# Performance work log

Measured on AMD Instinct MI355X. Metric: run time of the kernel, lower is better.

Reference implementation:

```python
import jax, jax.numpy as jnp
import numpy as np

NUM_HEADS = 16
NUM_GROUPS = 2
HEAD_DIM = 128  # in_features // num_heads = 2048 // 16
MAX_POS = 512 + 256 + 256  # MAX_SEQ_LEN + SHARED_SLOTS + OUTPUT_SLOTS


def _rope_tables():
    inv_freq = 1.0 / 10000 ** (jnp.arange(0, HEAD_DIM, 2) / HEAD_DIM)
    t = jnp.arange(MAX_POS)
    freqs = jnp.outer(t, inv_freq)
    freqs = jnp.concatenate([freqs, freqs], axis=-1)  # [MAX_POS, HEAD_DIM]
    return jnp.sin(freqs), jnp.cos(freqs)


def _rotate_half(x):
    h = x.shape[-1] // 2
    x1, x2 = x[..., :h], x[..., h:]
    return jnp.concatenate([-x2, x1], axis=-1)


def setup_inputs() -> dict:
    key = jax.random.key(0)
    ks = jax.random.split(key, 5)
    b, s, d = 4, 1024, 2048
    kvd = NUM_GROUPS * HEAD_DIM
    sc = 1.0 / np.sqrt(d).astype(np.float32)
    return {
        "x": jax.random.normal(ks[0], (b, s, d), jnp.float32),
        "Wq": jax.random.normal(ks[1], (d, d), jnp.float32) * sc,
        "bq": jnp.zeros((d,), jnp.float32),
        "Wk": jax.random.normal(ks[2], (d, kvd), jnp.float32) * sc,
        "bk": jnp.zeros((kvd,), jnp.float32),
        "Wv": jax.random.normal(ks[3], (d, kvd), jnp.float32) * sc,
        "bv": jnp.zeros((kvd,), jnp.float32),
        "Wo": jax.random.normal(ks[4], (d, d), jnp.float32) * sc,
        "bo": jnp.zeros((d,), jnp.float32),
    }


def reference(x, Wq, bq, Wk, bk, Wv, bv, Wo, bo):
    b, s, d = x.shape
    sin, cos = _rope_tables()
    # original: sin_cached[q_pos, None, :] broadcasts over (b, s, heads, head_dim)
    sin = sin[:s][None, :, None, :]
    cos = cos[:s][None, :, None, :]

    q = (x @ Wq + bq).reshape(b, s, NUM_HEADS, HEAD_DIM)
    k = (x @ Wk + bk).reshape(b, s, NUM_GROUPS, HEAD_DIM)
    v = (x @ Wv + bv).reshape(b, s, NUM_GROUPS, HEAD_DIM)

    q = q * cos + _rotate_half(q) * sin
    k = k * cos + _rotate_half(k) * sin

    # GQA: avoid materializing expanded K/V by grouping the head dim of q.
    r = NUM_HEADS // NUM_GROUPS  # repeats per group
    qg = q.reshape(b, s, NUM_GROUPS, r, HEAD_DIM)
    scale = HEAD_DIM ** -0.5
    scores = jnp.einsum('bsgrd,btgd->bgrst', qg, k) * scale
    attn = jax.nn.softmax(scores, axis=-1)
    out = jnp.einsum('bgrst,btgd->bsgrd', attn, v).reshape(b, s, d)
    return out @ Wo + bo
```

## Files before the change

### kernel.cpp

```cpp
#include <hip/hip_runtime.h>
#include <hip/hip_bf16.h>
#include <hip/hip_fp16.h>
#include <math.h>

#define BATCH   4
#define SEQ     1024
#define DMODEL  2048
#define NHEADS  16
#define NGROUPS 2
#define HDIM    128
#define ROWS    (BATCH * SEQ)
#define NQKV    2560

typedef float    f32x4 __attribute__((ext_vector_type(4)));
typedef _Float16 f16x8 __attribute__((ext_vector_type(8)));

__device__ __forceinline__ void glds16(const void* g, void* s) {
    __builtin_amdgcn_global_load_lds(
        (__attribute__((address_space(1))) void*)g,
        (__attribute__((address_space(3))) void*)s, 16, 0, 0);
}

__global__ void rope_table_kernel(float* __restrict__ sin_t, float* __restrict__ cos_t) {
    int idx = blockIdx.x * 256 + threadIdx.x;
    int p = idx >> 6, j = idx & 63;
    float inv = powf(10000.0f, -(float)j * (1.0f / 64.0f));
    float f = (float)p * inv;
    sin_t[idx] = sinf(f);
    cos_t[idx] = cosf(f);
}

__global__ void convert_x_kernel(const float* __restrict__ x, _Float16* __restrict__ xo) {
    int i = (blockIdx.x * 256 + threadIdx.x) * 8;
    float v[8];
    *reinterpret_cast<float4*>(&v[0]) = *reinterpret_cast<const float4*>(x + i);
    *reinterpret_cast<float4*>(&v[4]) = *reinterpret_cast<const float4*>(x + i + 4);
    f16x8 h;
#pragma unroll
    for (int j = 0; j < 8; ++j) h[j] = (_Float16)v[j];
    *reinterpret_cast<f16x8*>(xo + i) = h;
}

__global__ __launch_bounds__(256)
void transpose_w_kernel(const float* __restrict__ W, int ldw,
                        _Float16* __restrict__ dst, int drow0, int K) {
    __shared__ float tile[64][65];
    int n0 = blockIdx.x * 64, k0 = blockIdx.y * 64;
#pragma unroll
    for (int it = 0; it < 16; ++it) {
        int e = it * 256 + threadIdx.x;
        int r = e >> 6, c = e & 63;
        tile[r][c] = W[(size_t)(k0 + r) * ldw + n0 + c];
    }
    __syncthreads();
#pragma unroll
    for (int it = 0; it < 16; ++it) {
        int e = it * 256 + threadIdx.x;
        int nr = e >> 6, kc = e & 63;
        dst[(size_t)(drow0 + n0 + nr) * K + k0 + kc] = (_Float16)tile[kc][nr];
    }
}

__global__ void bias_cat_kernel(const float* __restrict__ bq, const float* __restrict__ bk,
                                const float* __restrict__ bv, float* __restrict__ bc) {
    int i = blockIdx.x * 256 + threadIdx.x;
    if (i >= NQKV) return;
    bc[i] = (i < 2048) ? bq[i] : ((i < 2304) ? bk[i - 2048] : bv[i - 2304]);
}

template<int OUT_HALF>
__global__ __launch_bounds__(256, 3)
void gemm_fp16_kernel(const _Float16* __restrict__ A, const _Float16* __restrict__ Bt,
                      const float* __restrict__ bias, void* __restrict__ Cout,
                      int M, int N, int K) {
    __shared__ __align__(16) _Float16 lds[16384];
    _Float16* As = lds;
    _Float16* Bs = lds + 8192;

    const int tid  = threadIdx.x;
    const int lane = tid & 63;
    const int w    = tid >> 6;
    const int nbn  = N >> 7;
    const int nwg  = gridDim.x;
    const int cpx  = nwg >> 3;
    const int bid  = blockIdx.x;
    const int swz  = (bid & 7) * cpx + (bid >> 3);
    const int row0 = (swz / nbn) << 7;
    const int col0 = (swz % nbn) << 7;
    const int wr   = (w >> 1) << 6;
    const int wc   = (w & 1) << 6;

    const f32x4 fz = {0.f, 0.f, 0.f, 0.f};
    f32x4 acc[4][4];
#pragma unroll
    for (int i = 0; i < 4; ++i)
#pragma unroll
        for (int j = 0; j < 4; ++j) acc[i][j] = fz;

    for (int k0 = 0; k0 < K; k0 += 64) {
        __syncthreads();
#pragma unroll
        for (int it = 0; it < 4; ++it) {
            int chunk = it * 256 + tid;
            int trow  = chunk >> 3;
            int jp    = chunk & 7;
            int j     = jp ^ (trow & 7);
            size_t aoff = (size_t)(row0 + trow) * K + k0 + j * 8;
            size_t boff = (size_t)(col0 + trow) * K + k0 + j * 8;
            int ldst = (it * 256 + (tid & 192)) * 16;
            glds16(A  + aoff, (char*)As + ldst);
            glds16(Bt + boff, (char*)Bs + ldst);
        }
        __syncthreads();

#pragma unroll
        for (int ks = 0; ks < 2; ++ks) {
            f16x8 a4[4], b4[4];
            int ja = ks * 4 + (lane >> 4);
#pragma unroll
            for (int i = 0; i < 4; ++i) {
                int ar = wr + i * 16 + (lane & 15);
                a4[i] = *reinterpret_cast<const f16x8*>(
                    (const char*)As + ar * 128 + ((ja ^ (ar & 7)) << 4));
                int br = wc + i * 16 + (lane & 15);
                b4[i] = *reinterpret_cast<const f16x8*>(
                    (const char*)Bs + br * 128 + ((ja ^ (br & 7)) << 4));
            }
#pragma unroll
            for (int i = 0; i < 4; ++i)
#pragma unroll
                for (int j = 0; j < 4; ++j)
                    acc[i][j] = __builtin_amdgcn_mfma_f32_16x16x32_f16(a4[i], b4[j], acc[i][j], 0, 0, 0);
        }
    }

    float bv4[4];
#pragma unroll
    for (int j = 0; j < 4; ++j) bv4[j] = bias[col0 + wc + j * 16 + (lane & 15)];
#pragma unroll
    for (int i = 0; i < 4; ++i)
#pragma unroll
        for (int j = 0; j < 4; ++j)
#pragma unroll
            for (int r = 0; r < 4; ++r) {
                int grow = row0 + wr + i * 16 + ((lane >> 4) << 2) + r;
                int gcol = col0 + wc + j * 16 + (lane & 15);
                float v = acc[i][j][r] + bv4[j];
                if (OUT_HALF)
                    ((_Float16*)Cout)[(size_t)grow * N + gcol] = (_Float16)v;
                else
                    ((float*)Cout)[(size_t)grow * N + gcol] = v;
            }
}

__global__ void rope_k_kernel(const _Float16* __restrict__ qkv,
                              const float* __restrict__ sin_t, const float* __restrict__ cos_t,
                              _Float16* __restrict__ kh) {
    int idx = blockIdx.x * 256 + threadIdx.x;
    int jc = idx & 7, t = idx >> 3;
    int j0 = jc * 8;
    int row = t >> 1, g = t & 1;
    int b = row >> 10, s = row & 1023;
    const _Float16* src = qkv + (size_t)row * NQKV + 2048 + g * HDIM;
    _Float16* dst = kh + ((size_t)(b * NGROUPS + g) * SEQ + s) * HDIM;
    f16x8 x1 = *reinterpret_cast<const f16x8*>(src + j0);
    f16x8 x2 = *reinterpret_cast<const f16x8*>(src + j0 + 64);
    float cc[8], ss[8];
    *reinterpret_cast<float4*>(&cc[0]) = *reinterpret_cast<const float4*>(cos_t + s * 64 + j0);
    *reinterpret_cast<float4*>(&cc[4]) = *reinterpret_cast<const float4*>(cos_t + s * 64 + j0 + 4);
    *reinterpret_cast<float4*>(&ss[0]) = *reinterpret_cast<const float4*>(sin_t + s * 64 + j0);
    *reinterpret_cast<float4*>(&ss[4]) = *reinterpret_cast<const float4*>(sin_t + s * 64 + j0 + 4);
    f16x8 o1, o2;
#pragma unroll
    for (int j = 0; j < 8; ++j) {
        float f1 = (float)x1[j], f2 = (float)x2[j];
        o1[j] = (_Float16)(f1 * cc[j] - f2 * ss[j]);
        o2[j] = (_Float16)(f2 * cc[j] + f1 * ss[j]);
    }
    *reinterpret_cast<f16x8*>(dst + j0)      = o1;
    *reinterpret_cast<f16x8*>(dst + j0 + 64) = o2;
}

__global__ __launch_bounds__(256)
void transpose_v_kernel(const _Float16* __restrict__ qkv, _Float16* __restrict__ vt) {
    __shared__ _Float16 tile[64][72];
    int s0 = blockIdx.x * 64, d0 = blockIdx.y * 64, bg = blockIdx.z;
    int b = bg >> 1, g = bg & 1;
#pragma unroll
    for (int it = 0; it < 2; ++it) {
        int c = it * 256 + threadIdx.x;
        int r = c >> 3, cc = (c & 7) * 8;
        f16x8 v = *reinterpret_cast<const f16x8*>(
            qkv + (size_t)(b * SEQ + s0 + r) * NQKV + 2304 + g * HDIM + d0 + cc);
#pragma unroll
        for (int j = 0; j < 8; ++j) tile[r][cc + j] = v[j];
    }
    __syncthreads();
#pragma unroll
    for (int it = 0; it < 2; ++it) {
        int c = it * 256 + threadIdx.x;
        int dr = c >> 3, sc = (c & 7) * 8;
        f16x8 o;
#pragma unroll
        for (int j = 0; j < 8; ++j) o[j] = tile[sc + j][dr];
        *reinterpret_cast<f16x8*>(vt + ((size_t)bg * HDIM + d0 + dr) * SEQ + s0 + sc) = o;
    }
}

__global__ __launch_bounds__(256, 2)
void attn_kernel(const _Float16* __restrict__ qkv, const _Float16* __restrict__ kh,
                 const _Float16* __restrict__ vt,
                 const float* __restrict__ sin_t, const float* __restrict__ cos_t,
                 _Float16* __restrict__ ao) {
    __shared__ __align__(16) char smem[73728];

    const int tid = threadIdx.x, lane = tid & 63, w = tid >> 6;
    const int qt0 = blockIdx.x << 6;
    const int h = blockIdx.y, b = blockIdx.z;
    const int g = h >> 3;
    const _Float16* kbase = kh + (size_t)(b * NGROUPS + g) * SEQ * HDIM;
    const _Float16* vbase = vt + (size_t)(b * NGROUPS + g) * HDIM * SEQ;

    {
        char* Kb = smem;
        char* Vb = smem + 16384;
#pragma unroll
        for (int it = 0; it < 4; ++it) {
            int c = it * 256 + tid;
            int row = c >> 4, jc = c & 15;
            int sj = jc ^ (row & 7);
            glds16((const char*)(kbase + (size_t)row * HDIM) + (sj << 4),
                   Kb + (it * 256 + (tid & 192)) * 16);
        }
#pragma unroll
        for (int it = 0; it < 4; ++it) {
            int c = it * 256 + tid;
            int d = c >> 3, jc = c & 7;
            int sj = jc ^ (d & 7);
            glds16((const char*)(vbase + (size_t)d * SEQ) + (sj << 4),
                   Vb + (it * 256 + (tid & 192)) * 16);
        }
    }

    const int srow = qt0 + w * 16 + (lane & 15);
    const int sl   = lane >> 4;
    const _Float16* qrp = qkv + (size_t)(b * SEQ + srow) * NQKV + h * HDIM;
    f16x8 af[4];
#pragma unroll
    for (int ks = 0; ks < 4; ++ks)
        af[ks] = *reinterpret_cast<const f16x8*>(qrp + (ks * 4 + sl) * 8);
    {
        const float qsc = 0.08838834764831845f;
#pragma unroll
        for (int ks = 0; ks < 2; ++ks) {
            int d0 = (ks * 4 + sl) * 8;
            float cc[8], ss[8];
            *reinterpret_cast<float4*>(&cc[0]) = *reinterpret_cast<const float4*>(cos_t + srow * 64 + d0);
            *reinterpret_cast<float4*>(&cc[4]) = *reinterpret_cast<const float4*>(cos_t + srow * 64 + d0 + 4);
            *reinterpret_cast<float4*>(&ss[0]) = *reinterpret_cast<const float4*>(sin_t + srow * 64 + d0);
            *reinterpret_cast<float4*>(&ss[4]) = *reinterpret_cast<const float4*>(sin_t + srow * 64 + d0 + 4);
#pragma unroll
            for (int j = 0; j < 8; ++j) {
                float f1 = (float)af[ks][j], f2 = (float)af[ks + 2][j];
                af[ks][j]     = (_Float16)((f1 * cc[j] - f2 * ss[j]) * qsc);
                af[ks + 2][j] = (_Float16)((f2 * cc[j] + f1 * ss[j]) * qsc);
            }
        }
    }

    float m_run[4] = {-1e30f, -1e30f, -1e30f, -1e30f};
    float l_run[4] = {0.f, 0.f, 0.f, 0.f};
    const f32x4 fz = {0.f, 0.f, 0.f, 0.f};
    f32x4 oacc[8];
#pragma unroll
    for (int i = 0; i < 8; ++i) oacc[i] = fz;

    char* Pw = smem + 65536 + w * 2048;
    const int prow = lane & 15;
    const int pswz = prow & 7;

    int cur = 0;
    for (int t = 0; t < SEQ / 64; ++t) {
        char* Kb = smem + (cur << 15);
        char* Vb = Kb + 16384;
        if (t < SEQ / 64 - 1) {
            char* Kn = smem + ((cur ^ 1) << 15);
            char* Vn = Kn + 16384;
            int t0n = (t + 1) << 6;
#pragma unroll
            for (int it = 0; it < 4; ++it) {
                int c = it * 256 + tid;
                int row = c >> 4, jc = c & 15;
                int sj = jc ^ (row & 7);
                glds16((const char*)(kbase + (size_t)(t0n + row) * HDIM) + (sj << 4),
                       Kn + (it * 256 + (tid & 192)) * 16);
            }
#pragma unroll
            for (int it = 0; it < 4; ++it) {
                int c = it * 256 + tid;
                int d = c >> 3, jc = c & 7;
                int sj = jc ^ (d & 7);
                glds16((const char*)(vbase + (size_t)d * SEQ + t0n) + (sj << 4),
                       Vn + (it * 256 + (tid & 192)) * 16);
            }
            asm volatile("s_waitcnt vmcnt(8)" ::: "memory");
        } else {
            asm volatile("s_waitcnt vmcnt(0)" ::: "memory");
        }
        asm volatile("s_barrier" ::: "memory");

        f32x4 sacc[4];
#pragma unroll
        for (int i = 0; i < 4; ++i) sacc[i] = fz;
#pragma unroll
        for (int ks = 0; ks < 4; ++ks) {
#pragma unroll
            for (int nf = 0; nf < 4; ++nf) {
                int trow = nf * 16 + (lane & 15);
                f16x8 bf = *reinterpret_cast<const f16x8*>(
                    Kb + trow * 256 + (((ks * 4 + (lane >> 4)) ^ (trow & 7)) << 4));
                sacc[nf] = __builtin_amdgcn_mfma_f32_16x16x32_f16(af[ks], bf, sacc[nf], 0, 0, 0);
            }
        }

        float pm[4];
#pragma unroll
        for (int r = 0; r < 4; ++r) {
            float v = fmaxf(fmaxf(sacc[0][r], sacc[1][r]), fmaxf(sacc[2][r], sacc[3][r]));
            v = fmaxf(v, __shfl_xor(v, 1, 16));
            v = fmaxf(v, __shfl_xor(v, 2, 16));
            v = fmaxf(v, __shfl_xor(v, 4, 16));
            v = fmaxf(v, __shfl_xor(v, 8, 16));
            pm[r] = v;
        }
        float growth = fmaxf(fmaxf(pm[0] - m_run[0], pm[1] - m_run[1]),
                             fmaxf(pm[2] - m_run[2], pm[3] - m_run[3]));
        if (__any(growth > 8.0f)) {
            float scl[4];
#pragma unroll
            for (int r = 0; r < 4; ++r) {
                float mn = fmaxf(m_run[r], pm[r]);
                scl[r] = __expf(m_run[r] - mn);
                m_run[r] = mn;
                l_run[r] *= scl[r];
            }
#pragma unroll
            for (int i = 0; i < 8; ++i) {
                f32x4 o = oacc[i];
                o[0] *= scl[0]; o[1] *= scl[1]; o[2] *= scl[2]; o[3] *= scl[3];
                oacc[i] = o;
            }
        }
        float psum[4] = {0.f, 0.f, 0.f, 0.f};
#pragma unroll
        for (int nf = 0; nf < 4; ++nf)
#pragma unroll
            for (int r = 0; r < 4; ++r) {
                float p = __expf(sacc[nf][r] - m_run[r]);
                sacc[nf][r] = p;
                psum[r] += p;
            }
#pragma unroll
        for (int r = 0; r < 4; ++r) {
            float ps = psum[r];
            ps += __shfl_xor(ps, 1, 16);
            ps += __shfl_xor(ps, 2, 16);
            ps += __shfl_xor(ps, 4, 16);
            ps += __shfl_xor(ps, 8, 16);
            l_run[r] += ps;
        }

#pragma unroll
        for (int nf = 0; nf < 4; ++nf)
#pragma unroll
            for (int r = 0; r < 4; ++r) {
                int pr = ((lane >> 4) << 2) + r;
                int pc = nf * 16 + (lane & 15);
                int byte = pr * 128 + ((pc * 2) ^ ((pr & 7) << 4));
                *reinterpret_cast<_Float16*>(Pw + byte) = (_Float16)sacc[nf][r];
            }

#pragma unroll
        for (int ks = 0; ks < 2; ++ks) {
            int chP = ks * 4 + (lane >> 4);
            f16x8 pa = *reinterpret_cast<const f16x8*>(Pw + prow * 128 + ((chP ^ pswz) << 4));
#pragma unroll
            for (int nf = 0; nf < 8; ++nf) {
                int vrow = nf * 16 + (lane & 15);
                f16x8 vf = *reinterpret_cast<const f16x8*>(
                    Vb + vrow * 128 + (((ks * 4 + (lane >> 4)) ^ (vrow & 7)) << 4));
                oacc[nf] = __builtin_amdgcn_mfma_f32_16x16x32_f16(pa, vf, oacc[nf], 0, 0, 0);
            }
        }

        asm volatile("s_barrier" ::: "memory");
        cur ^= 1;
    }

#pragma unroll
    for (int nf = 0; nf < 8; ++nf)
#pragma unroll
        for (int r = 0; r < 4; ++r) {
            int qr  = qt0 + w * 16 + ((lane >> 4) << 2) + r;
            int col = h * HDIM + nf * 16 + (lane & 15);
            float v = oacc[nf][r] / l_run[r];
            ao[(size_t)(b * SEQ + qr) * DMODEL + col] = (_Float16)v;
        }
}

extern "C" void kernel_launch(void* const* d_in, const int* in_sizes, int n_in,
                              void* d_out, int out_size, void* d_ws, size_t ws_size,
                              hipStream_t stream) {
    const float* x  = (const float*)d_in[0];
    const float* Wq = (const float*)d_in[1];
    const float* bq = (const float*)d_in[2];
    const float* Wk = (const float*)d_in[3];
    const float* bk = (const float*)d_in[4];
    const float* Wv = (const float*)d_in[5];
    const float* bv = (const float*)d_in[6];
    const float* Wo = (const float*)d_in[7];
    const float* bo = (const float*)d_in[8];
    float* out = (float*)d_out;

    char* ws = (char*)d_ws;
    _Float16* xs     = (_Float16*)(ws);
    _Float16* wqkv16 = (_Float16*)(ws + 16777216);
    _Float16* wot16  = (_Float16*)(ws + 27262976);
    _Float16* qkv16  = (_Float16*)(ws + 35651584);
    _Float16* khb    = (_Float16*)(ws + 56623104);
    _Float16* vtb    = (_Float16*)(ws + 58720256);
    float*    sint   = (float*)(ws + 60817408);
    float*    cost   = (float*)(ws + 61079552);
    float*    bias_c = (float*)(ws + 61341696);
    _Float16* ao = xs;

    rope_table_kernel<<<SEQ * 64 / 256, 256, 0, stream>>>(sint, cost);
    convert_x_kernel<<<ROWS * DMODEL / 8 / 256, 256, 0, stream>>>(x, xs);
    transpose_w_kernel<<<dim3(32, 32), 256, 0, stream>>>(Wq, DMODEL, wqkv16, 0, DMODEL);
    transpose_w_kernel<<<dim3(4, 32),  256, 0, stream>>>(Wk, 256,    wqkv16, 2048, DMODEL);
    transpose_w_kernel<<<dim3(4, 32),  256, 0, stream>>>(Wv, 256,    wqkv16, 2304, DMODEL);
    transpose_w_kernel<<<dim3(32, 32), 256, 0, stream>>>(Wo, DMODEL, wot16,  0, DMODEL);
    bias_cat_kernel<<<10, 256, 0, stream>>>(bq, bk, bv, bias_c);

    gemm_fp16_kernel<1><<<(ROWS / 128) * (NQKV / 128), 256, 0, stream>>>(
        xs, wqkv16, bias_c, qkv16, ROWS, NQKV, DMODEL);

    rope_k_kernel<<<(ROWS * NGROUPS * 8) / 256, 256, 0, stream>>>(qkv16, sint, cost, khb);
    transpose_v_kernel<<<dim3(SEQ / 64, HDIM / 64, BATCH * NGROUPS), 256, 0, stream>>>(qkv16, vtb);

    attn_kernel<<<dim3(SEQ / 64, NHEADS, BATCH), 256, 0, stream>>>(
        qkv16, khb, vtb, sint, cost, ao);

    gemm_fp16_kernel<0><<<(ROWS / 128) * (DMODEL / 128), 256, 0, stream>>>(
        ao, wot16, bo, out, ROWS, DMODEL, DMODEL);
}
```

Measured before the change: 318.9 us.

## Process 32 query rows per wave in attention and use DPP row reductions

Each attention block now covers 128 query rows, with each wave holding two 16-row Q fragments, so every K and V fragment read from LDS feeds two MFMAs. The grid is halved and the per-wave P buffer is doubled in size. The 16-lane max and sum reductions now use DPP moves instead of shuffles. In exchange, the larger accumulator set raises register pressure, and the smaller grid may reduce occupancy and SM coverage.

```diff
diff --git a/kernel.cpp b/kernel.cpp
--- a/kernel.cpp
+++ b/kernel.cpp
@@ -19,6 +19,21 @@
     __builtin_amdgcn_global_load_lds(
         (__attribute__((address_space(1))) void*)g,
         (__attribute__((address_space(3))) void*)s, 16, 0, 0);
+}
+
+__device__ __forceinline__ float red16_max(float v) {
+    v = fmaxf(v, __int_as_float(__builtin_amdgcn_mov_dpp(__float_as_int(v), 0xB1, 0xF, 0xF, true)));
+    v = fmaxf(v, __int_as_float(__builtin_amdgcn_mov_dpp(__float_as_int(v), 0x4E, 0xF, 0xF, true)));
+    v = fmaxf(v, __int_as_float(__builtin_amdgcn_mov_dpp(__float_as_int(v), 0x124, 0xF, 0xF, true)));
+    v = fmaxf(v, __int_as_float(__builtin_amdgcn_mov_dpp(__float_as_int(v), 0x128, 0xF, 0xF, true)));
+    return v;
+}
+__device__ __forceinline__ float red16_sum(float v) {
+    v += __int_as_float(__builtin_amdgcn_mov_dpp(__float_as_int(v), 0xB1, 0xF, 0xF, true));
+    v += __int_as_float(__builtin_amdgcn_mov_dpp(__float_as_int(v), 0x4E, 0xF, 0xF, true));
+    v += __int_as_float(__builtin_amdgcn_mov_dpp(__float_as_int(v), 0x124, 0xF, 0xF, true));
+    v += __int_as_float(__builtin_amdgcn_mov_dpp(__float_as_int(v), 0x128, 0xF, 0xF, true));
+    return v;
 }
 
 __global__ void rope_table_kernel(float* __restrict__ sin_t, float* __restrict__ cos_t) {
@@ -212,10 +227,10 @@
                  const _Float16* __restrict__ vt,
                  const float* __restrict__ sin_t, const float* __restrict__ cos_t,
                  _Float16* __restrict__ ao) {
-    __shared__ __align__(16) char smem[73728];
+    __shared__ __align__(16) char smem[81920];
 
     const int tid = threadIdx.x, lane = tid & 63, w = tid >> 6;
-    const int qt0 = blockIdx.x << 6;
+    const int qt0 = blockIdx.x << 7;
     const int h = blockIdx.y, b = blockIdx.z;
     const int g = h >> 3;
     const _Float16* kbase = kh + (size_t)(b * NGROUPS + g) * SEQ * HDIM;
@@ -242,14 +257,15 @@
         }
     }
 
-    const int srow = qt0 + w * 16 + (lane & 15);
-    const int sl   = lane >> 4;
-    const _Float16* qrp = qkv + (size_t)(b * SEQ + srow) * NQKV + h * HDIM;
-    f16x8 af[4];
-#pragma unroll
-    for (int ks = 0; ks < 4; ++ks)
-        af[ks] = *reinterpret_cast<const f16x8*>(qrp + (ks * 4 + sl) * 8);
-    {
+    const int sl = lane >> 4;
+    f16x8 af[2][4];
+#pragma unroll
+    for (int m = 0; m < 2; ++m) {
+        int srow = qt0 + w * 32 + m * 16 + (lane & 15);
+        const _Float16* qrp = qkv + (size_t)(b * SEQ + srow) * NQKV + h * HDIM;
+#pragma unroll
+        for (int ks = 0; ks < 4; ++ks)
+            af[m][ks] = *reinterpret_cast<const f16x8*>(qrp + (ks * 4 + sl) * 8);
         const float qsc = 0.08838834764831845f;
 #pragma unroll
         for (int ks = 0; ks < 2; ++ks) {
@@ -261,23 +277,27 @@
             *reinterpret_cast<float4*>(&ss[4]) = *reinterpret_cast<const float4*>(sin_t + srow * 64 + d0 + 4);
 #pragma unroll
             for (int j = 0; j < 8; ++j) {
-                float f1 = (float)af[ks][j], f2 = (float)af[ks + 2][j];
-                af[ks][j]     = (_Float16)((f1 * cc[j] - f2 * ss[j]) * qsc);
-                af[ks + 2][j] = (_Float16)((f2 * cc[j] + f1 * ss[j]) * qsc);
-            }
-        }
-    }
-
-    float m_run[4] = {-1e30f, -1e30f, -1e30f, -1e30f};
-    float l_run[4] = {0.f, 0.f, 0.f, 0.f};
+                float f1 = (float)af[m][ks][j], f2 = (float)af[m][ks + 2][j];
+                af[m][ks][j]     = (_Float16)((f1 * cc[j] - f2 * ss[j]) * qsc);
+                af[m][ks + 2][j] = (_Float16)((f2 * cc[j] + f1 * ss[j]) * qsc);
+            }
+        }
+    }
+
+    float m_run[2][4], l_run[2][4];
+#pragma unroll
+    for (int m = 0; m < 2; ++m)
+#pragma unroll
+        for (int r = 0; r < 4; ++r) { m_run[m][r] = -1e30f; l_run[m][r] = 0.f; }
     const f32x4 fz = {0.f, 0.f, 0.f, 0.f};
-    f32x4 oacc[8];
-#pragma unroll
-    for (int i = 0; i < 8; ++i) oacc[i] = fz;
-
-    char* Pw = smem + 65536 + w * 2048;
+    f32x4 oacc[2][8];
+#pragma unroll
+    for (int m = 0; m < 2; ++m)
+#pragma unroll
+        for (int i = 0; i < 8; ++i) oacc[m][i] = fz;
+
+    char* Pw = smem + 65536 + w * 4096;
     const int prow = lane & 15;
-    const int pswz = prow & 7;
 
     int cur = 0;
     for (int t = 0; t < SEQ / 64; ++t) {
@@ -309,9 +329,11 @@
         }
         asm volatile("s_barrier" ::: "memory");
 
-        f32x4 sacc[4];
-#pragma unroll
-        for (int i = 0; i < 4; ++i) sacc[i] = fz;
+        f32x4 sacc[2][4];
+#pragma unroll
+        for (int m = 0; m < 2; ++m)
+#pragma unroll
+            for (int i = 0; i < 4; ++i) sacc[m][i] = fz;
 #pragma unroll
         for (int ks = 0; ks < 4; ++ks) {
 #pragma unroll
@@ -319,77 +341,85 @@
                 int trow = nf * 16 + (lane & 15);
                 f16x8 bf = *reinterpret_cast<const f16x8*>(
                     Kb + trow * 256 + (((ks * 4 + (lane >> 4)) ^ (trow & 7)) << 4));
-                sacc[nf] = __builtin_amdgcn_mfma_f32_16x16x32_f16(af[ks], bf, sacc[nf], 0, 0, 0);
-            }
-        }
-
-        float pm[4];
-#pragma unroll
-        for (int r = 0; r < 4; ++r) {
-            float v = fmaxf(fmaxf(sacc[0][r], sacc[1][r]), fmaxf(sacc[2][r], sacc[3][r]));
-            v = fmaxf(v, __shfl_xor(v, 1, 16));
-            v = fmaxf(v, __shfl_xor(v, 2, 16));
-            v = fmaxf(v, __shfl_xor(v, 4, 16));
-            v = fmaxf(v, __shfl_xor(v, 8, 16));
-            pm[r] = v;
-        }
-        float growth = fmaxf(fmaxf(pm[0] - m_run[0], pm[1] - m_run[1]),
-                             fmaxf(pm[2] - m_run[2], pm[3] - m_run[3]));
+                sacc[0][nf] = __builtin_amdgcn_mfma_f32_16x16x32_f16(af[0][ks], bf, sacc[0][nf], 0, 0, 0);
+                sacc[1][nf] = __builtin_amdgcn_mfma_f32_16x16x32_f16(af[1][ks], bf, sacc[1][nf], 0, 0, 0);
+            }
+        }
+
+        float pm[2][4];
+        float growth = -1e30f;
+#pragma unroll
+        for (int m = 0; m < 2; ++m)
+#pragma unroll
+            for (int r = 0; r < 4; ++r) {
+                float v = fmaxf(fmaxf(sacc[m][0][r], sacc[m][1][r]),
+                                fmaxf(sacc[m][2][r], sacc[m][3][r]));
+                v = red16_max(v);
+                pm[m][r] = v;
+                growth = fmaxf(growth, v - m_run[m][r]);
+            }
         if (__any(growth > 8.0f)) {
-            float scl[4];
+            float scl[2][4];
+#pragma unroll
+            for (int m = 0; m < 2; ++m)
+#pragma unroll
+                for (int r = 0; r < 4; ++r) {
+                    float mn = fmaxf(m_run[m][r], pm[m][r]);
+                    scl[m][r] = __expf(m_run[m][r] - mn);
+                    m_run[m][r] = mn;
+                    l_run[m][r] *= scl[m][r];
+                }
+#pragma unroll
+            for (int m = 0; m < 2; ++m)
+#pragma unroll
+                for (int i = 0; i < 8; ++i) {
+                    f32x4 o = oacc[m][i];
+                    o[0] *= scl[m][0]; o[1] *= scl[m][1];
+                    o[2] *= scl[m][2]; o[3] *= scl[m][3];
+                    oacc[m][i] = o;
+                }
+        }
+#pragma unroll
+        for (int m = 0; m < 2; ++m)
 #pragma unroll
             for (int r = 0; r < 4; ++r) {
-                float mn = fmaxf(m_run[r], pm[r]);
-                scl[r] = __expf(m_run[r] - mn);
-                m_run[r] = mn;
-                l_run[r] *= scl[r];
-            }
-#pragma unroll
-            for (int i = 0; i < 8; ++i) {
-                f32x4 o = oacc[i];
-                o[0] *= scl[0]; o[1] *= scl[1]; o[2] *= scl[2]; o[3] *= scl[3];
-                oacc[i] = o;
-            }
-        }
-        float psum[4] = {0.f, 0.f, 0.f, 0.f};
-#pragma unroll
-        for (int nf = 0; nf < 4; ++nf)
-#pragma unroll
-            for (int r = 0; r < 4; ++r) {
-                float p = __expf(sacc[nf][r] - m_run[r]);
-                sacc[nf][r] = p;
-                psum[r] += p;
-            }
-#pragma unroll
-        for (int r = 0; r < 4; ++r) {
-            float ps = psum[r];
-            ps += __shfl_xor(ps, 1, 16);
-            ps += __shfl_xor(ps, 2, 16);
-            ps += __shfl_xor(ps, 4, 16);
-            ps += __shfl_xor(ps, 8, 16);
-            l_run[r] += ps;
-        }
-
-#pragma unroll
-        for (int nf = 0; nf < 4; ++nf)
-#pragma unroll
-            for (int r = 0; r < 4; ++r) {
-                int pr = ((lane >> 4) << 2) + r;
-                int pc = nf * 16 + (lane & 15);
-                int byte = pr * 128 + ((pc * 2) ^ ((pr & 7) << 4));
-                *reinterpret_cast<_Float16*>(Pw + byte) = (_Float16)sacc[nf][r];
-            }
+                float ps = 0.f;
+#pragma unroll
+                for (int nf = 0; nf < 4; ++nf) {
+                    float p = __expf(sacc[m][nf][r] - m_run[m][r]);
+                    sacc[m][nf][r] = p;
+                    ps += p;
+                }
+                l_run[m][r] += red16_sum(ps);
+            }
+
+#pragma unroll
+        for (int m = 0; m < 2; ++m)
+#pragma unroll
+            for (int nf = 0; nf < 4; ++nf)
+#pragma unroll
+                for (int r = 0; r < 4; ++r) {
+                    int pr = m * 16 + ((lane >> 4) << 2) + r;
+                    int pc = nf * 16 + (lane & 15);
+                    int byte = pr * 128 + ((pc * 2) ^ ((pr & 7) << 4));
+                    *reinterpret_cast<_Float16*>(Pw + byte) = (_Float16)sacc[m][nf][r];
+                }
 
 #pragma unroll
         for (int ks = 0; ks < 2; ++ks) {
             int chP = ks * 4 + (lane >> 4);
-            f16x8 pa = *reinterpret_cast<const f16x8*>(Pw + prow * 128 + ((chP ^ pswz) << 4));
+            f16x8 pa[2];
+#pragma unroll
+            for (int m = 0; m < 2; ++m)
+                pa[m] = *reinterpret_cast<const f16x8*>(
+                    Pw + (m * 16 + prow) * 128 + ((chP ^ (prow & 7)) << 4));
 #pragma unroll
             for (int nf = 0; nf < 8; ++nf) {
                 int vrow = nf * 16 + (lane & 15);
                 f16x8 vf = *reinterpret_cast<const f16x8*>(
                     Vb + vrow * 128 + (((ks * 4 + (lane >> 4)) ^ (vrow & 7)) << 4));
-                oacc[nf] = __builtin_amdgcn_mfma_f32_16x16x32_f16(pa, vf, oacc[nf], 0, 0, 0);
+                oacc[0][nf] = __builtin_amdgcn_mfma_f32_16x16x32_f16(pa[0], vf, oacc[0][nf], 0, 0, 0);
+                oacc[1][nf] = __builtin_amdgcn_mfma_f32_16x16x32_f16(pa[1], vf, oacc[1][nf], 0, 0, 0);
             }
         }
 
@@ -398,14 +428,16 @@
     }
 
 #pragma unroll
-    for (int nf = 0; nf < 8; ++nf)
-#pragma unroll
-        for (int r = 0; r < 4; ++r) {
-            int qr  = qt0 + w * 16 + ((lane >> 4) << 2) + r;
-            int col = h * HDIM + nf * 16 + (lane & 15);
-            float v = oacc[nf][r] / l_run[r];
-            ao[(size_t)(b * SEQ + qr) * DMODEL + col] = (_Float16)v;
-        }
+    for (int m = 0; m < 2; ++m)
+#pragma unroll
+        for (int nf = 0; nf < 8; ++nf)
+#pragma unroll
+            for (int r = 0; r < 4; ++r) {
+                int qr  = qt0 + w * 32 + m * 16 + ((lane >> 4) << 2) + r;
+                int col = h * HDIM + nf * 16 + (lane & 15);
+                float v = oacc[m][nf][r] / l_run[m][r];
+                ao[(size_t)(b * SEQ + qr) * DMODEL + col] = (_Float16)v;
+            }
 }
 
 extern "C" void kernel_launch(void* const* d_in, const int* in_sizes, int n_in,
@@ -448,7 +480,7 @@
     rope_k_kernel<<<(ROWS * NGROUPS * 8) / 256, 256, 0, stream>>>(qkv16, sint, cost, khb);
     transpose_v_kernel<<<dim3(SEQ / 64, HDIM / 64, BATCH * NGROUPS), 256, 0, stream>>>(qkv16, vtb);
 
-    attn_kernel<<<dim3(SEQ / 64, NHEADS, BATCH), 256, 0, stream>>>(
+    attn_kernel<<<dim3(SEQ / 128, NHEADS, BATCH), 256, 0, stream>>>(
         qkv16, khb, vtb, sint, cost, ao);
 
     gemm_fp16_kernel<0><<<(ROWS / 128) * (DMODEL / 128), 256, 0, stream>>>(
```

Result: faster. 293.4 us (-8.0%).
